# Kernel optimization log

Hardware: AMD Instinct MI355X
Metric: run time of the kernel (lower is better)

## Reference

```python
import jax, jax.numpy as jnp
import numpy as np

B, T, D = 8, 4096, 512
Q, K = 4, 1024
KERNEL, STRIDE = 5, 2
COMMIT = 0.25


def setup_inputs() -> dict:
    key = jax.random.key(0)
    k1, k2, k3 = jax.random.split(key, 3)
    x = jax.random.normal(k1, (B, T, D), dtype=jnp.float32)
    codebooks = jax.random.normal(k2, (Q, K, D), dtype=jnp.float32)
    # he_normal fan_in = KERNEL * D
    conv_w = jax.random.normal(k3, (KERNEL, D, D), dtype=jnp.float32) * np.sqrt(2.0 / (KERNEL * D))
    return {"x": x, "codebooks": codebooks, "conv_w": conv_w}


def _vq_nearest(residual, cb):
    # residual: [B,T,D], cb: [K,D] -> squared L2 distances [B,T,K]
    d = (jnp.sum(residual * residual, axis=-1, keepdims=True)
         - 2.0 * jnp.einsum('btd,kd->btk', residual, cb)
         + jnp.sum(cb * cb, axis=-1))
    idx = jnp.argmin(d, axis=-1)          # [B,T] int
    q = cb[idx]                            # [B,T,D] gather
    return q, idx


def residual_vq(x, codebooks):
    residual = x
    quantized_out = jnp.zeros_like(x)
    losses = []
    indices = []
    for qi in range(Q):  # small fixed number of quantizers
        q, idx = _vq_nearest(residual, codebooks[qi])
        # commitment loss (codebook frozen at inference / EMA-updated in training)
        losses.append(COMMIT * jnp.mean((jax.lax.stop_gradient(q) - residual) ** 2))
        # straight-through estimator
        q_st = residual + jax.lax.stop_gradient(q - residual)
        quantized_out = quantized_out + q_st
        residual = residual - jax.lax.stop_gradient(q)
        indices.append(idx)
    loss = jnp.sum(jnp.stack(losses))
    return quantized_out, jnp.stack(indices, axis=0), loss


def reference(x, codebooks, conv_w):
    quantized_out, indices, vq_loss = residual_vq(x, codebooks)
    # Conv1D, stride 2, 'same' padding, no bias: NWC x WIO -> NWC
    y = jax.lax.conv_general_dilated(
        quantized_out, conv_w,
        window_strides=(STRIDE,), padding='SAME',
        dimension_numbers=('NWC', 'WIO', 'NWC'))
    y = jax.nn.gelu(y, approximate=False)
    return y, quantized_out, indices, vq_loss
```

## Files before the change

### kernel.cpp

```cpp
#include <hip/hip_runtime.h>
#include <math.h>

#define Bq 8
#define Tq 4096
#define Dq 512
#define Qn 4
#define Kk 1024
#define OWn 2048
#define NROWS (Bq*Tq)

#define QO_OFF (Bq*OWn*Dq)
#define IDX_OFF (QO_OFF + Bq*Tq*Dq)
#define LOSS_OFF (IDX_OFF + Qn*NROWS)

typedef __bf16 bf16x8 __attribute__((ext_vector_type(8)));
typedef _Float16 f16x8 __attribute__((ext_vector_type(8)));
typedef float f32x16 __attribute__((ext_vector_type(16)));
typedef float f32x4 __attribute__((ext_vector_type(4)));

__device__ __forceinline__ unsigned pack2h(_Float16 a, _Float16 b) {
  return (unsigned)__builtin_bit_cast(unsigned short, a)
       | ((unsigned)__builtin_bit_cast(unsigned short, b) << 16);
}

__global__ __launch_bounds__(256) void prep_cb(const float* __restrict__ cb,
                                               float* __restrict__ cbnorm,
                                               _Float16* __restrict__ cbf,
                                               float* __restrict__ lacc) {
  int w = threadIdx.x >> 6, lane = threadIdx.x & 63;
  int row = blockIdx.x * 4 + w;
  int q = row >> 10, k = row & 1023;
  const f32x4* c4 = (const f32x4*)(cb + (size_t)row * Dq);
  f32x4 v0 = c4[lane * 2], v1 = c4[lane * 2 + 1];
  float s = v0.x*v0.x + v0.y*v0.y + v0.z*v0.z + v0.w*v0.w
          + v1.x*v1.x + v1.y*v1.y + v1.z*v1.z + v1.w*v1.w;
  f16x8 bv;
  bv[0]=(_Float16)v0.x; bv[1]=(_Float16)v0.y; bv[2]=(_Float16)v0.z; bv[3]=(_Float16)v0.w;
  bv[4]=(_Float16)v1.x; bv[5]=(_Float16)v1.y; bv[6]=(_Float16)v1.z; bv[7]=(_Float16)v1.w;
  int ds = lane >> 1, hs = lane & 1;
  size_t off = ((size_t)((k >> 5) * 32 + ds) * 2 + hs) * 256 + (k & 31) * 8;
  *(f16x8*)(cbf + (size_t)q * (Kk * Dq) + off) = bv;
#pragma unroll
  for (int off2 = 32; off2; off2 >>= 1) s += __shfl_down(s, off2);
  if (lane == 0) cbnorm[row] = s;
  if (blockIdx.x == 0 && threadIdx.x == 0) *lacc = 0.f;
}

__global__ __launch_bounds__(256) void prep_cmax(const float* __restrict__ cbnorm,
                                                 float* __restrict__ cmax) {
  int w = threadIdx.x >> 6, lane = threadIdx.x & 63;
  float m = 0.f;
#pragma unroll
  for (int j = 0; j < 16; ++j) m = fmaxf(m, cbnorm[w * Kk + lane * 16 + j]);
#pragma unroll
  for (int off = 32; off; off >>= 1) m = fmaxf(m, __shfl_down(m, off));
  if (lane == 0) cmax[w] = sqrtf(m);
}

__global__ __launch_bounds__(256) void prep_wb(const float* __restrict__ w,
                                               __bf16* __restrict__ wb) {
  int g = blockIdx.x * 256 + threadIdx.x;
  int l31 = g & 31, hs = (g >> 5) & 1, c32 = (g >> 6) & 15, s = g >> 10;
  int kw = s >> 5, ci16 = s & 31;
  int ci = ci16 * 16 + hs * 8;
  int co = c32 * 32 + l31;
  bf16x8 bv;
#pragma unroll
  for (int e = 0; e < 8; ++e)
    bv[e] = (__bf16)w[(size_t)(kw * Dq + ci + e) * Dq + co];
  *(bf16x8*)(wb + (size_t)g * 8) = bv;
}

__global__ __launch_bounds__(1024, 1) void vq_all(
    const float* __restrict__ x, float* __restrict__ qo,
    const _Float16* __restrict__ cbf, const float* __restrict__ cb,
    const float* __restrict__ cbnorm, const float* __restrict__ cmax,
    float* __restrict__ idxo, float* __restrict__ lacc) {
  __shared__ _Float16 rh[64 * 512];
  __shared__ unsigned redB[64 * 8];
  __shared__ float rnorm_l[64];
  __shared__ float thrL[64];
  __shared__ int rowcount[64];
  __shared__ unsigned short rowlist[64 * 32];

  const int tid = threadIdx.x;
  const int w = tid >> 6, lane = tid & 63, l31 = lane & 31, hs = lane >> 5;
  const int row0g = blockIdx.x * 64;
  char* rhc = (char*)rh;

  f32x4 r0[4], r1[4];
#pragma unroll
  for (int rr = 0; rr < 4; ++rr) {
    size_t gb = (size_t)(row0g + w * 4 + rr) * Dq + lane * 8;
    r0[rr] = *(const f32x4*)(x + gb);
    r1[rr] = *(const f32x4*)(x + gb + 4);
  }
  float lsum = 0.f;

#pragma unroll 1
  for (int qi = 0; qi < Qn; ++qi) {
    const _Float16* cbf_q = cbf + (size_t)qi * (Kk * Dq);
    const float*    cb_q  = cb  + (size_t)qi * (Kk * Dq);
    const float*    cbn_q = cbnorm + qi * Kk;

#pragma unroll
    for (int rr = 0; rr < 4; ++rr) {
      int row = w * 4 + rr;
      f16x8 bv;
      bv[0]=(_Float16)r0[rr].x; bv[1]=(_Float16)r0[rr].y;
      bv[2]=(_Float16)r0[rr].z; bv[3]=(_Float16)r0[rr].w;
      bv[4]=(_Float16)r1[rr].x; bv[5]=(_Float16)r1[rr].y;
      bv[6]=(_Float16)r1[rr].z; bv[7]=(_Float16)r1[rr].w;
      *(f16x8*)(rhc + ((row * 1024 + lane * 16) ^ ((row & 7) << 4))) = bv;
      float rn = r0[rr].x*r0[rr].x + r0[rr].y*r0[rr].y + r0[rr].z*r0[rr].z + r0[rr].w*r0[rr].w
               + r1[rr].x*r1[rr].x + r1[rr].y*r1[rr].y + r1[rr].z*r1[rr].z + r1[rr].w*r1[rr].w;
#pragma unroll
      for (int off = 1; off < 64; off <<= 1) rn += __shfl_xor(rn, off);
      if (lane == 0) rnorm_l[row] = rn;
    }
    __syncthreads();

    unsigned ps[4][8];
    const int cg = w & 7, rg = w >> 3;
    const int ab0 = (rg * 32 + l31) * 1024 + hs * 16;
    const int asw = (l31 & 7) << 4;
#pragma unroll
    for (int p = 0; p < 2; ++p) {
      const int ct0 = 2 * p, ct1 = 2 * p + 1;
      const _Float16* bp0 = cbf_q + (size_t)(cg * 4 + ct0) * 16384 + hs * 256 + l31 * 8;
      const _Float16* bp1 = cbf_q + (size_t)(cg * 4 + ct1) * 16384 + hs * 256 + l31 * 8;
      f32x16 accA, accB;
#pragma unroll
      for (int i = 0; i < 16; ++i) { accA[i] = 0.f; accB[i] = 0.f; }
#pragma unroll 8
      for (int ds = 0; ds < 32; ++ds) {
        f16x8 a  = *(const f16x8*)(rhc + ((ab0 + ds * 32) ^ asw));
        f16x8 b0 = *(const f16x8*)(bp0 + ds * 512);
        f16x8 b1 = *(const f16x8*)(bp1 + ds * 512);
        accA = __builtin_amdgcn_mfma_f32_32x32x16_f16(a, b0, accA, 0, 0, 0);
        accB = __builtin_amdgcn_mfma_f32_32x32x16_f16(a, b1, accB, 0, 0, 0);
      }
      const float cn0 = cbn_q[cg * 128 + ct0 * 32 + l31];
      const float cn1 = cbn_q[cg * 128 + ct1 * 32 + l31];
#pragma unroll
      for (int j = 0; j < 8; ++j) {
        ps[ct0][j] = pack2h((_Float16)(cn0 - 2.f * accA[2*j]), (_Float16)(cn0 - 2.f * accA[2*j+1]));
        ps[ct1][j] = pack2h((_Float16)(cn1 - 2.f * accB[2*j]), (_Float16)(cn1 - 2.f * accB[2*j+1]));
      }
    }

    {
      unsigned pk[16];
#pragma unroll
      for (int i = 0; i < 16; ++i) {
        pk[i] = 0xFFFFFFFFu;
#pragma unroll
        for (int ct = 0; ct < 4; ++ct) {
          unsigned col = (unsigned)(cg * 128 + ct * 32 + l31);
          unsigned u = (ps[ct][i >> 1] >> ((i & 1) * 16)) & 0xFFFFu;
          unsigned key = (u & 0x8000u) ? (u ^ 0xFFFFu) : (u | 0x8000u);
          unsigned pkc = (key << 10) | col;
          if (pkc < pk[i]) pk[i] = pkc;
        }
#pragma unroll
        for (int off = 1; off <= 16; off <<= 1) {
          unsigned t = __shfl_xor(pk[i], off);
          if (t < pk[i]) pk[i] = t;
        }
      }
      if (l31 == 0) {
#pragma unroll
        for (int i = 0; i < 16; ++i) {
          int rit = rg * 32 + (i & 3) + 8 * (i >> 2) + 4 * hs;
          redB[rit * 8 + cg] = pk[i];
        }
      }
    }
    __syncthreads();

    if (tid < 64) {
      unsigned mb = redB[tid * 8];
#pragma unroll
      for (int j = 1; j < 8; ++j) {
        unsigned v = redB[tid * 8 + j];
        if (v < mb) mb = v;
      }
      unsigned key = (mb >> 10) & 0xFFFFu;
      unsigned ub = (key & 0x8000u) ? (key ^ 0x8000u) : (key ^ 0xFFFFu);
      float mstar = (float)__builtin_bit_cast(_Float16, (unsigned short)ub);
      float rn = sqrtf(rnorm_l[tid]);
      float cm = cmax[qi];
      thrL[tid] = mstar + 0.005f * rn * cm + 0.001f * fabsf(mstar) + 0.3f;
      rowcount[tid] = 0;
    }
    __syncthreads();

#pragma unroll
    for (int i = 0; i < 16; ++i) {
      int rit = rg * 32 + (i & 3) + 8 * (i >> 2) + 4 * hs;
      float t = thrL[rit];
#pragma unroll
      for (int ct = 0; ct < 4; ++ct) {
        unsigned col = (unsigned)(cg * 128 + ct * 32 + l31);
        unsigned u = (ps[ct][i >> 1] >> ((i & 1) * 16)) & 0xFFFFu;
        float s = (float)__builtin_bit_cast(_Float16, (unsigned short)u);
        if (s <= t) {
          int p = atomicAdd(&rowcount[rit], 1);
          if (p < 32) rowlist[rit * 32 + p] = (unsigned short)col;
        }
      }
    }
    __syncthreads();

#pragma unroll
    for (int rr = 0; rr < 4; ++rr) {
      int row = w * 4 + rr;
      int cnt = rowcount[row];
      int total = (cnt > 32) ? Kk : cnt;
      float bs = 3.4028235e38f; int bk = 1 << 30;
      for (int ci2 = 0; ci2 < total; ++ci2) {
        int k = (cnt > 32) ? ci2 : (int)rowlist[row * 32 + ci2];
        const f32x4* crow = (const f32x4*)(cb_q + ((size_t)k << 9)) + lane * 2;
        f32x4 c0 = crow[0], c1 = crow[1];
        float dot = 0.f;
        dot = fmaf(r0[rr].x, c0.x, dot); dot = fmaf(r0[rr].y, c0.y, dot);
        dot = fmaf(r0[rr].z, c0.z, dot); dot = fmaf(r0[rr].w, c0.w, dot);
        dot = fmaf(r1[rr].x, c1.x, dot); dot = fmaf(r1[rr].y, c1.y, dot);
        dot = fmaf(r1[rr].z, c1.z, dot); dot = fmaf(r1[rr].w, c1.w, dot);
#pragma unroll
        for (int off = 1; off < 64; off <<= 1) dot += __shfl_xor(dot, off);
        float sc = cbn_q[k] - 2.f * dot;
        if (sc < bs || (sc == bs && k < bk)) { bs = sc; bk = k; }
      }
      if (lane == 0) idxo[(size_t)qi * NROWS + row0g + row] = (float)bk;
      const f32x4* crow = (const f32x4*)(cb_q + ((size_t)bk << 9)) + lane * 2;
      f32x4 c0 = crow[0], c1 = crow[1];
      r0[rr].x -= c0.x; r0[rr].y -= c0.y; r0[rr].z -= c0.z; r0[rr].w -= c0.w;
      r1[rr].x -= c1.x; r1[rr].y -= c1.y; r1[rr].z -= c1.z; r1[rr].w -= c1.w;
      lsum += r0[rr].x*r0[rr].x + r0[rr].y*r0[rr].y + r0[rr].z*r0[rr].z + r0[rr].w*r0[rr].w
            + r1[rr].x*r1[rr].x + r1[rr].y*r1[rr].y + r1[rr].z*r1[rr].z + r1[rr].w*r1[rr].w;
    }
    __syncthreads();
  }

#pragma unroll
  for (int rr = 0; rr < 4; ++rr) {
    size_t gb = (size_t)(row0g + w * 4 + rr) * Dq + lane * 8;
    f32x4 xv0 = *(const f32x4*)(x + gb), xv1 = *(const f32x4*)(x + gb + 4);
    f32x4 o0, o1;
    o0.x = xv0.x - r0[rr].x; o0.y = xv0.y - r0[rr].y;
    o0.z = xv0.z - r0[rr].z; o0.w = xv0.w - r0[rr].w;
    o1.x = xv1.x - r1[rr].x; o1.y = xv1.y - r1[rr].y;
    o1.z = xv1.z - r1[rr].z; o1.w = xv1.w - r1[rr].w;
    *(f32x4*)(qo + gb) = o0;
    *(f32x4*)(qo + gb + 4) = o1;
  }
#pragma unroll
  for (int off = 1; off < 64; off <<= 1) lsum += __shfl_xor(lsum, off);
  if (lane == 0) atomicAdd(lacc, lsum);
}

__global__ __launch_bounds__(512, 2) void conv_mfma(const float* __restrict__ qo,
                                                    const __bf16* __restrict__ wb,
                                                    float* __restrict__ y) {
  __shared__ char As[259 * 128];
  const int tid = threadIdx.x;
  const int w = tid >> 6, lane = tid & 63, l31 = lane & 31, hs = lane >> 5;
  const int rowblk = blockIdx.x, coblk = blockIdx.y;
  const int n = rowblk >> 4;
  const int o0 = (rowblk & 15) * 128;
  const int t0 = 2 * o0 - 1;
  const int c32g = coblk * 8 + w;

  f32x16 acc[4];
#pragma unroll
  for (int rt = 0; rt < 4; ++rt)
#pragma unroll
    for (int i = 0; i < 16; ++i) acc[rt][i] = 0.f;

  for (int ct8 = 0; ct8 < 8; ++ct8) {
    __syncthreads();
    for (int s = tid; s < 2072; s += 512) {
      int irow = s >> 3, cg = s & 7;
      int t = t0 + irow;
      bf16x8 bv;
      if (t >= 0 && t < Tq) {
        const float* src = qo + ((size_t)(n * Tq + t)) * Dq + ct8 * 64 + cg * 8;
        f32x4 v0 = *(const f32x4*)(src), v1 = *(const f32x4*)(src + 4);
        bv[0]=(__bf16)v0.x; bv[1]=(__bf16)v0.y; bv[2]=(__bf16)v0.z; bv[3]=(__bf16)v0.w;
        bv[4]=(__bf16)v1.x; bv[5]=(__bf16)v1.y; bv[6]=(__bf16)v1.z; bv[7]=(__bf16)v1.w;
      } else {
#pragma unroll
        for (int e = 0; e < 8; ++e) bv[e] = (__bf16)0.f;
      }
      *(bf16x8*)(As + ((irow * 128 + cg * 16) ^ (((irow >> 1) & 7) << 4))) = bv;
    }
    __syncthreads();
#pragma unroll
    for (int kw = 0; kw < 5; ++kw) {
#pragma unroll
      for (int ks = 0; ks < 4; ++ks) {
        int s16 = kw * 32 + ct8 * 4 + ks;
        bf16x8 b = *(const bf16x8*)(wb + ((size_t)(s16 * 16 + c32g) * 2 + hs) * 256 + l31 * 8);
#pragma unroll
        for (int rt = 0; rt < 4; ++rt) {
          int ir = 2 * (rt * 32 + l31) + kw;
          bf16x8 a = *(const bf16x8*)(As + ((ir * 128 + ks * 32 + hs * 16) ^ (((ir >> 1) & 7) << 4)));
          acc[rt] = __builtin_amdgcn_mfma_f32_32x32x16_bf16(a, b, acc[rt], 0, 0, 0);
        }
      }
    }
  }
  const int co = coblk * 256 + w * 32 + l31;
#pragma unroll
  for (int rt = 0; rt < 4; ++rt)
#pragma unroll
    for (int i = 0; i < 16; ++i) {
      int orow = rt * 32 + (i & 3) + 8 * (i >> 2) + 4 * hs;
      float v = acc[rt][i];
      float g = 0.5f * v * (1.f + erff(v * 0.70710678118654752f));
      y[((size_t)(n * OWn + o0 + orow)) * Dq + co] = g;
    }
}

__global__ void loss_final(const float* __restrict__ lacc, float* __restrict__ out) {
  out[0] = 0.25f * lacc[0] / 16777216.0f;
}

extern "C" void kernel_launch(void* const* d_in, const int* in_sizes, int n_in,
                              void* d_out, int out_size, void* d_ws, size_t ws_size,
                              hipStream_t stream) {
  const float* x  = (const float*)d_in[0];
  const float* cb = (const float*)d_in[1];
  const float* cw = (const float*)d_in[2];
  float* out = (float*)d_out;
  float* y    = out;
  float* qo   = out + QO_OFF;
  float* idxo = out + IDX_OFF;
  float* losso = out + LOSS_OFF;

  float* fws    = (float*)d_ws;
  float* lacc   = fws;
  float* cmax   = fws + 8;
  float* cbnorm = fws + 16;
  _Float16* cbf = (_Float16*)((char*)d_ws + (32 << 10));
  __bf16* wb  = (__bf16*)((char*)d_ws + (8 << 20));

  prep_cb<<<1024, 256, 0, stream>>>(cb, cbnorm, cbf, lacc);
  prep_cmax<<<1, 256, 0, stream>>>(cbnorm, cmax);
  prep_wb<<<640, 256, 0, stream>>>(cw, wb);

  vq_all<<<512, 1024, 0, stream>>>(x, qo, cbf, cb, cbnorm, cmax, idxo, lacc);

  conv_mfma<<<dim3(128, 2), 512, 0, stream>>>(qo, wb, y);
  loss_final<<<1, 1, 0, stream>>>(lacc, losso);
}
```

Baseline: 596.1 us.

## Stage VQ score matrix in LDS and do per-row argmin with 32-row blocks

Shrinks the VQ block from 64 rows/1024 threads to 32 rows/512 threads, with each wave covering all rows of a 128-column slice. Half-precision scores go to an LDS score matrix instead of being packed in registers. Each wave then reads its own rows to find the minimum, threshold and candidates, replacing the cross-wave packed-key reduction and two barriers. An exact fp32 rescoring is skipped when only one candidate survives. The cost is more LDS traffic and a different occupancy and launch shape.

New measurement: 500.1 us. 1.19x faster.

```diff
diff --git a/kernel.cpp b/kernel.cpp
--- a/kernel.cpp
+++ b/kernel.cpp
@@ -8,6 +8,7 @@
 #define Kk 1024
 #define OWn 2048
 #define NROWS (Bq*Tq)
+#define SSTR 1032
 
 #define QO_OFF (Bq*OWn*Dq)
 #define IDX_OFF (QO_OFF + Bq*Tq*Dq)
@@ -17,11 +18,6 @@
 typedef _Float16 f16x8 __attribute__((ext_vector_type(8)));
 typedef float f32x16 __attribute__((ext_vector_type(16)));
 typedef float f32x4 __attribute__((ext_vector_type(4)));
-
-__device__ __forceinline__ unsigned pack2h(_Float16 a, _Float16 b) {
-  return (unsigned)__builtin_bit_cast(unsigned short, a)
-       | ((unsigned)__builtin_bit_cast(unsigned short, b) << 16);
-}
 
 __global__ __launch_bounds__(256) void prep_cb(const float* __restrict__ cb,
                                                float* __restrict__ cbnorm,
@@ -71,21 +67,19 @@
   *(bf16x8*)(wb + (size_t)g * 8) = bv;
 }
 
-__global__ __launch_bounds__(1024, 1) void vq_all(
+__global__ __launch_bounds__(512, 1) void vq_all(
     const float* __restrict__ x, float* __restrict__ qo,
     const _Float16* __restrict__ cbf, const float* __restrict__ cb,
     const float* __restrict__ cbnorm, const float* __restrict__ cmax,
     float* __restrict__ idxo, float* __restrict__ lacc) {
-  __shared__ _Float16 rh[64 * 512];
-  __shared__ unsigned redB[64 * 8];
-  __shared__ float rnorm_l[64];
-  __shared__ float thrL[64];
-  __shared__ int rowcount[64];
-  __shared__ unsigned short rowlist[64 * 32];
+  __shared__ _Float16 rh[32 * 512];
+  __shared__ _Float16 Sh[32 * SSTR];
+  __shared__ int rowcount[32];
+  __shared__ unsigned short rowlist[32 * 32];
 
   const int tid = threadIdx.x;
   const int w = tid >> 6, lane = tid & 63, l31 = lane & 31, hs = lane >> 5;
-  const int row0g = blockIdx.x * 64;
+  const int row0g = blockIdx.x * 32;
   char* rhc = (char*)rh;
 
   f32x4 r0[4], r1[4];
@@ -102,7 +96,9 @@
     const _Float16* cbf_q = cbf + (size_t)qi * (Kk * Dq);
     const float*    cb_q  = cb  + (size_t)qi * (Kk * Dq);
     const float*    cbn_q = cbnorm + qi * Kk;
-
+    const float cm = cmax[qi];
+
+    float rnf[4];
 #pragma unroll
     for (int rr = 0; rr < 4; ++rr) {
       int row = w * 4 + rr;
@@ -116,121 +112,87 @@
                + r1[rr].x*r1[rr].x + r1[rr].y*r1[rr].y + r1[rr].z*r1[rr].z + r1[rr].w*r1[rr].w;
 #pragma unroll
       for (int off = 1; off < 64; off <<= 1) rn += __shfl_xor(rn, off);
-      if (lane == 0) rnorm_l[row] = rn;
-    }
-    __syncthreads();
-
-    unsigned ps[4][8];
-    const int cg = w & 7, rg = w >> 3;
-    const int ab0 = (rg * 32 + l31) * 1024 + hs * 16;
+      rnf[rr] = rn;
+      if (lane == 0) rowcount[row] = 0;
+    }
+    __syncthreads();
+
+    const int ab0 = l31 * 1024 + hs * 16;
     const int asw = (l31 & 7) << 4;
-#pragma unroll
+#pragma unroll 1
     for (int p = 0; p < 2; ++p) {
-      const int ct0 = 2 * p, ct1 = 2 * p + 1;
-      const _Float16* bp0 = cbf_q + (size_t)(cg * 4 + ct0) * 16384 + hs * 256 + l31 * 8;
-      const _Float16* bp1 = cbf_q + (size_t)(cg * 4 + ct1) * 16384 + hs * 256 + l31 * 8;
-      f32x16 accA, accB;
-#pragma unroll
-      for (int i = 0; i < 16; ++i) { accA[i] = 0.f; accB[i] = 0.f; }
+      const int cb0 = w * 128 + 2 * p * 32;
+      const _Float16* bp0 = cbf_q + (size_t)(w * 4 + 2 * p) * 16384 + hs * 256 + l31 * 8;
+      const _Float16* bp1 = bp0 + 16384;
+      f32x16 acc0, acc1;
+#pragma unroll
+      for (int i = 0; i < 16; ++i) { acc0[i] = 0.f; acc1[i] = 0.f; }
 #pragma unroll 8
       for (int ds = 0; ds < 32; ++ds) {
         f16x8 a  = *(const f16x8*)(rhc + ((ab0 + ds * 32) ^ asw));
         f16x8 b0 = *(const f16x8*)(bp0 + ds * 512);
         f16x8 b1 = *(const f16x8*)(bp1 + ds * 512);
-        accA = __builtin_amdgcn_mfma_f32_32x32x16_f16(a, b0, accA, 0, 0, 0);
-        accB = __builtin_amdgcn_mfma_f32_32x32x16_f16(a, b1, accB, 0, 0, 0);
-      }
-      const float cn0 = cbn_q[cg * 128 + ct0 * 32 + l31];
-      const float cn1 = cbn_q[cg * 128 + ct1 * 32 + l31];
-#pragma unroll
-      for (int j = 0; j < 8; ++j) {
-        ps[ct0][j] = pack2h((_Float16)(cn0 - 2.f * accA[2*j]), (_Float16)(cn0 - 2.f * accA[2*j+1]));
-        ps[ct1][j] = pack2h((_Float16)(cn1 - 2.f * accB[2*j]), (_Float16)(cn1 - 2.f * accB[2*j+1]));
-      }
-    }
-
-    {
-      unsigned pk[16];
+        acc0 = __builtin_amdgcn_mfma_f32_32x32x16_f16(a, b0, acc0, 0, 0, 0);
+        acc1 = __builtin_amdgcn_mfma_f32_32x32x16_f16(a, b1, acc1, 0, 0, 0);
+      }
+      const float cn0 = cbn_q[cb0 + l31];
+      const float cn1 = cbn_q[cb0 + 32 + l31];
 #pragma unroll
       for (int i = 0; i < 16; ++i) {
-        pk[i] = 0xFFFFFFFFu;
-#pragma unroll
-        for (int ct = 0; ct < 4; ++ct) {
-          unsigned col = (unsigned)(cg * 128 + ct * 32 + l31);
-          unsigned u = (ps[ct][i >> 1] >> ((i & 1) * 16)) & 0xFFFFu;
-          unsigned key = (u & 0x8000u) ? (u ^ 0xFFFFu) : (u | 0x8000u);
-          unsigned pkc = (key << 10) | col;
-          if (pkc < pk[i]) pk[i] = pkc;
-        }
-#pragma unroll
-        for (int off = 1; off <= 16; off <<= 1) {
-          unsigned t = __shfl_xor(pk[i], off);
-          if (t < pk[i]) pk[i] = t;
-        }
-      }
-      if (l31 == 0) {
-#pragma unroll
-        for (int i = 0; i < 16; ++i) {
-          int rit = rg * 32 + (i & 3) + 8 * (i >> 2) + 4 * hs;
-          redB[rit * 8 + cg] = pk[i];
-        }
-      }
-    }
-    __syncthreads();
-
-    if (tid < 64) {
-      unsigned mb = redB[tid * 8];
-#pragma unroll
-      for (int j = 1; j < 8; ++j) {
-        unsigned v = redB[tid * 8 + j];
-        if (v < mb) mb = v;
-      }
-      unsigned key = (mb >> 10) & 0xFFFFu;
-      unsigned ub = (key & 0x8000u) ? (key ^ 0x8000u) : (key ^ 0xFFFFu);
-      float mstar = (float)__builtin_bit_cast(_Float16, (unsigned short)ub);
-      float rn = sqrtf(rnorm_l[tid]);
-      float cm = cmax[qi];
-      thrL[tid] = mstar + 0.005f * rn * cm + 0.001f * fabsf(mstar) + 0.3f;
-      rowcount[tid] = 0;
-    }
-    __syncthreads();
-
-#pragma unroll
-    for (int i = 0; i < 16; ++i) {
-      int rit = rg * 32 + (i & 3) + 8 * (i >> 2) + 4 * hs;
-      float t = thrL[rit];
-#pragma unroll
-      for (int ct = 0; ct < 4; ++ct) {
-        unsigned col = (unsigned)(cg * 128 + ct * 32 + l31);
-        unsigned u = (ps[ct][i >> 1] >> ((i & 1) * 16)) & 0xFFFFu;
-        float s = (float)__builtin_bit_cast(_Float16, (unsigned short)u);
-        if (s <= t) {
-          int p = atomicAdd(&rowcount[rit], 1);
-          if (p < 32) rowlist[rit * 32 + p] = (unsigned short)col;
-        }
-      }
-    }
-    __syncthreads();
-
-#pragma unroll
+        int rit = (i & 3) + 8 * (i >> 2) + 4 * hs;
+        Sh[rit * SSTR + cb0 + l31]      = (_Float16)(cn0 - 2.f * acc0[i]);
+        Sh[rit * SSTR + cb0 + 32 + l31] = (_Float16)(cn1 - 2.f * acc1[i]);
+      }
+    }
+    __syncthreads();
+
+#pragma unroll 1
     for (int rr = 0; rr < 4; ++rr) {
       int row = w * 4 + rr;
+      const _Float16* srow = Sh + row * SSTR;
+      f16x8 sv0 = *(const f16x8*)(srow + lane * 16);
+      f16x8 sv1 = *(const f16x8*)(srow + lane * 16 + 8);
+      float m = 3.4028235e38f;
+#pragma unroll
+      for (int j = 0; j < 8; ++j) {
+        m = fminf(m, (float)sv0[j]);
+        m = fminf(m, (float)sv1[j]);
+      }
+#pragma unroll
+      for (int off = 1; off < 64; off <<= 1) m = fminf(m, __shfl_xor(m, off));
+      float thr = m + 0.005f * sqrtf(rnf[rr]) * cm + 0.001f * fabsf(m) + 0.3f;
+#pragma unroll
+      for (int j = 0; j < 8; ++j) {
+        if ((float)sv0[j] <= thr) {
+          int p = atomicAdd(&rowcount[row], 1);
+          if (p < 32) rowlist[row * 32 + p] = (unsigned short)(lane * 16 + j);
+        }
+        if ((float)sv1[j] <= thr) {
+          int p = atomicAdd(&rowcount[row], 1);
+          if (p < 32) rowlist[row * 32 + p] = (unsigned short)(lane * 16 + 8 + j);
+        }
+      }
       int cnt = rowcount[row];
-      int total = (cnt > 32) ? Kk : cnt;
-      float bs = 3.4028235e38f; int bk = 1 << 30;
-      for (int ci2 = 0; ci2 < total; ++ci2) {
-        int k = (cnt > 32) ? ci2 : (int)rowlist[row * 32 + ci2];
-        const f32x4* crow = (const f32x4*)(cb_q + ((size_t)k << 9)) + lane * 2;
-        f32x4 c0 = crow[0], c1 = crow[1];
-        float dot = 0.f;
-        dot = fmaf(r0[rr].x, c0.x, dot); dot = fmaf(r0[rr].y, c0.y, dot);
-        dot = fmaf(r0[rr].z, c0.z, dot); dot = fmaf(r0[rr].w, c0.w, dot);
-        dot = fmaf(r1[rr].x, c1.x, dot); dot = fmaf(r1[rr].y, c1.y, dot);
-        dot = fmaf(r1[rr].z, c1.z, dot); dot = fmaf(r1[rr].w, c1.w, dot);
-#pragma unroll
-        for (int off = 1; off < 64; off <<= 1) dot += __shfl_xor(dot, off);
-        float sc = cbn_q[k] - 2.f * dot;
-        if (sc < bs || (sc == bs && k < bk)) { bs = sc; bk = k; }
+      int bk;
+      if (cnt == 1) {
+        bk = (int)rowlist[row * 32];
+      } else {
+        int total = (cnt > 32) ? Kk : cnt;
+        float bs = 3.4028235e38f; bk = 1 << 30;
+        for (int ci2 = 0; ci2 < total; ++ci2) {
+          int k = (cnt > 32) ? ci2 : (int)rowlist[row * 32 + ci2];
+          const f32x4* crow = (const f32x4*)(cb_q + ((size_t)k << 9)) + lane * 2;
+          f32x4 c0 = crow[0], c1 = crow[1];
+          float dot = 0.f;
+          dot = fmaf(r0[rr].x, c0.x, dot); dot = fmaf(r0[rr].y, c0.y, dot);
+          dot = fmaf(r0[rr].z, c0.z, dot); dot = fmaf(r0[rr].w, c0.w, dot);
+          dot = fmaf(r1[rr].x, c1.x, dot); dot = fmaf(r1[rr].y, c1.y, dot);
+          dot = fmaf(r1[rr].z, c1.z, dot); dot = fmaf(r1[rr].w, c1.w, dot);
+#pragma unroll
+          for (int off = 1; off < 64; off <<= 1) dot += __shfl_xor(dot, off);
+          float sc = cbn_q[k] - 2.f * dot;
+          if (sc < bs || (sc == bs && k < bk)) { bs = sc; bk = k; }
+        }
       }
       if (lane == 0) idxo[(size_t)qi * NROWS + row0g + row] = (float)bk;
       const f32x4* crow = (const f32x4*)(cb_q + ((size_t)bk << 9)) + lane * 2;
@@ -350,7 +312,7 @@
   prep_cmax<<<1, 256, 0, stream>>>(cbnorm, cmax);
   prep_wb<<<640, 256, 0, stream>>>(cw, wb);
 
-  vq_all<<<512, 1024, 0, stream>>>(x, qo, cbf, cb, cbnorm, cmax, idxo, lacc);
+  vq_all<<<1024, 512, 0, stream>>>(x, qo, cbf, cb, cbnorm, cmax, idxo, lacc);
 
   conv_mfma<<<dim3(128, 2), 512, 0, stream>>>(qo, wb, y);
   loss_final<<<1, 1, 0, stream>>>(lacc, losso);
```
